# Optimization experiments

Measured on AMD Instinct MI355X. Metric: run time of the kernel, lower is better.

Reference implementation:

```python
import jax, jax.numpy as jnp
import numpy as np

B, S, IN_DIM, OUT_DIM = 4, 2048, 1024, 1024
NEG = -9e15

def _xavier(key, shape, gain=1.414):
    fan_in, fan_out = shape[0], shape[1]
    a = gain * np.sqrt(6.0 / (fan_in + fan_out))
    return jax.random.uniform(key, shape, jnp.float32, -a, a)

def setup_inputs() -> dict:
    key = jax.random.key(0)
    ks = jax.random.split(key, 8)
    x = jax.random.normal(ks[0], (B, S, IN_DIM), jnp.float32)
    W_query = _xavier(ks[1], (IN_DIM, OUT_DIM))
    W_key = _xavier(ks[2], (IN_DIM, OUT_DIM))
    W_value = _xavier(ks[3], (IN_DIM, OUT_DIM))
    # torch Linear default init (kaiming-uniform-ish); values don't matter for correctness baseline
    W1 = _xavier(ks[4], (OUT_DIM + IN_DIM, OUT_DIM), gain=1.0)
    b1 = jnp.zeros((OUT_DIM,), jnp.float32)
    W2 = _xavier(ks[5], (OUT_DIM, OUT_DIM), gain=1.0)
    b2 = jnp.zeros((OUT_DIM,), jnp.float32)
    return {"x": x, "W_query": W_query, "W_key": W_key, "W_value": W_value,
            "W1": W1, "b1": b1, "W2": W2, "b2": b2}

def reference(x, W_query, W_key, W_value, W1, b1, W2, b2):
    # QKV projections: [B,S,in] @ [in,out] -> [B,S,out]
    q = jnp.einsum('bsi,io->bso', x, W_query)
    k = jnp.einsum('bsi,io->bso', x, W_key)
    v = jnp.einsum('bsi,io->bso', x, W_value)
    scale = 1.0 / jnp.sqrt(jnp.float32(OUT_DIM))
    e = jnp.einsum('bqd,bkd->bqk', q, k) * scale  # [B,S,S]
    causal = jnp.tril(jnp.ones((S, S), jnp.float32))  # mask > 0 keeps lower triangle
    attn = jnp.where(causal > 0, e, jnp.float32(NEG))
    attn = jax.nn.softmax(attn, axis=2)
    # dropout: eval mode (train=False) -> identity
    out = jnp.einsum('bqk,bkd->bqd', attn, v)  # [B,S,out]
    h = jnp.concatenate([out, x], axis=-1)  # [B,S,out+in]
    h = jax.nn.relu(jnp.einsum('bsf,fo->bso', h, W1) + b1)
    return jnp.einsum('bsf,fo->bso', h, W2) + b2
```

## Files before the change

kernel.cpp:

```cpp
#include <hip/hip_runtime.h>
#include <stdint.h>

typedef __attribute__((ext_vector_type(8))) short short8;
typedef __attribute__((ext_vector_type(4))) short short4v;
typedef __attribute__((ext_vector_type(4))) float f32x4;

__device__ __forceinline__ unsigned short f32_to_bf16(float f) {
    unsigned int u = __float_as_uint(f);
    u += 0x7FFFu + ((u >> 16) & 1u);
    return (unsigned short)(u >> 16);
}

__device__ __forceinline__ short8 load8_f32_as_bf16(const float* __restrict__ ap) {
    f32x4 f0 = *(const f32x4*)ap;
    f32x4 f1 = *(const f32x4*)(ap + 4);
    union { short8 s; unsigned short u[8]; } cv;
#pragma unroll
    for (int t = 0; t < 4; ++t) {
        cv.u[t]     = f32_to_bf16(f0[t]);
        cv.u[t + 4] = f32_to_bf16(f1[t]);
    }
    return cv.s;
}

__device__ __forceinline__ void gld_lds16(const void* g, void* l) {
    __builtin_amdgcn_global_load_lds(
        (const __attribute__((address_space(1))) unsigned int*)(unsigned long long)(uintptr_t)g,
        (__attribute__((address_space(3))) unsigned int*)(unsigned int)(uintptr_t)l,
        16, 0, 0);
}

template<int MT>
__global__ __launch_bounds__(256, 4)
void gemm128(const unsigned short* __restrict__ A,
             int lda,
             const unsigned short* __restrict__ B, int ldb,
             void* __restrict__ C, int ldc, int K,
             long bStride, long cStride)
{
    int z = blockIdx.z;
    int mblk = blockIdx.x * 8 + (blockIdx.y & 7);
    int nblk = blockIdx.y >> 3;
    int m0 = mblk * MT;
    int n0 = nblk * 128;

    const unsigned short* Ab = A;
    const unsigned short* Bb = B + (size_t)z * bStride;

    __shared__ __align__(16) short As[MT * 64];
    __shared__ __align__(16) short Bs[128 * 64];

    int tid  = threadIdx.x;
    int lane = tid & 63, wid = tid >> 6;
    constexpr int MI = MT / 32;
    int wm = (wid & 1) * (MT / 2), wn = (wid >> 1) * 64;
    int fr = lane & 15, fq = lane >> 4;
    int sw0 = ((fq    ) ^ (fr & 7)) * 16;
    int sw1 = ((fq ^ 4) ^ (fr & 7)) * 16;

    int rS = tid >> 3;
    int cS = ((tid & 7) ^ (rS & 7)) * 8;
    char* AsB = (char*)As; char* BsB = (char*)Bs;

    f32x4 acc[MI][4];
#pragma unroll
    for (int i = 0; i < MI; ++i)
#pragma unroll
    for (int j = 0; j < 4; ++j) acc[i][j] = f32x4{0.f, 0.f, 0.f, 0.f};

    for (int k0 = 0; k0 < K; k0 += 64) {
        const unsigned short* pa = Ab + (size_t)(m0 + rS) * lda + k0 + cS;
        const unsigned short* pb = Bb + (size_t)(n0 + rS) * ldb + k0 + cS;
#pragma unroll
        for (int t = 0; t < MT / 32; ++t)
            gld_lds16(pa + (size_t)(32 * t) * lda, AsB + t * 4096 + tid * 16);
#pragma unroll
        for (int t = 0; t < 4; ++t)
            gld_lds16(pb + (size_t)(32 * t) * ldb,  BsB + t * 4096 + tid * 16);
        __syncthreads();

#pragma unroll
        for (int kh = 0; kh < 2; ++kh) {
            int sw = kh ? sw1 : sw0;
            short8 a[MI], b[4];
#pragma unroll
            for (int i = 0; i < MI; ++i)
                a[i] = *(const short8*)(AsB + (wm + i * 16 + fr) * 128 + sw);
#pragma unroll
            for (int j = 0; j < 4; ++j)
                b[j] = *(const short8*)(BsB + (wn + j * 16 + fr) * 128 + sw);
#pragma unroll
            for (int i = 0; i < MI; ++i)
#pragma unroll
            for (int j = 0; j < 4; ++j)
                acc[i][j] = __builtin_amdgcn_mfma_f32_16x16x32_bf16(a[i], b[j], acc[i][j], 0, 0, 0);
        }
        __syncthreads();
    }

    unsigned short* Cz = (unsigned short*)C + (size_t)z * cStride;
#pragma unroll
    for (int i = 0; i < MI; ++i)
#pragma unroll
    for (int j = 0; j < 4; ++j)
#pragma unroll
    for (int r = 0; r < 4; ++r) {
        int row = m0 + wm + i * 16 + fq * 4 + r;
        int col = n0 + wn + j * 16 + fr;
        Cz[(size_t)row * ldc + col] = f32_to_bf16(acc[i][j][r]);
    }
}

__global__ __launch_bounds__(256, 4)
void scorevt(const unsigned short* __restrict__ q,
             const unsigned short* __restrict__ k,
             unsigned short* __restrict__ S, float* __restrict__ rsum,
             float scale,
             const unsigned short* __restrict__ WvT,
             const unsigned short* __restrict__ xb,
             unsigned short* __restrict__ vT)
{
    int glin = blockIdx.x;
    bool isV = glin >= 544;
    int z = 0, m0, n0;
    const unsigned short *Ab, *Bb;
    if (!isV) {
        int t = (glin & 7) * 68 + (glin >> 3);
        z = t / 136;
        int tri = t - z * 136;
        int a = (int)sqrtf(2.f * (float)tri + 1.f);
        if (a > 15) a = 15;
        while (a < 15 && ((a + 1) * (a + 2) / 2) <= tri) ++a;
        while (a > 0 && (a * (a + 1) / 2) > tri) --a;
        m0 = a * 128;
        n0 = (tri - a * (a + 1) / 2) * 128;
        Ab = q + (size_t)z * 2048 * 1024;
        Bb = k + (size_t)z * 2048 * 1024;
    } else {
        int g2 = glin - 544;
        int xcd = g2 & 7, idx = g2 >> 3;
        int nblk = xcd * 8 + (idx & 7);
        int mblk = idx >> 3;
        m0 = mblk * 128;
        n0 = nblk * 128;
        Ab = WvT;
        Bb = xb;
    }

    __shared__ __align__(16) short As[128 * 64];
    __shared__ __align__(16) short Bs[128 * 64];

    int tid  = threadIdx.x;
    int lane = tid & 63, wid = tid >> 6;
    int wm = (wid & 1) * 64, wn = (wid >> 1) * 64;
    int fr = lane & 15, fq = lane >> 4;
    int sw0 = ((fq    ) ^ (fr & 7)) * 16;
    int sw1 = ((fq ^ 4) ^ (fr & 7)) * 16;

    int rS = tid >> 3;
    int cS = ((tid & 7) ^ (rS & 7)) * 8;
    char* AsB = (char*)As; char* BsB = (char*)Bs;

    f32x4 acc[4][4];
#pragma unroll
    for (int i = 0; i < 4; ++i)
#pragma unroll
    for (int j = 0; j < 4; ++j) acc[i][j] = f32x4{0.f, 0.f, 0.f, 0.f};

    for (int k0 = 0; k0 < 1024; k0 += 64) {
        const unsigned short* pa = Ab + (size_t)(m0 + rS) * 1024 + k0 + cS;
        const unsigned short* pb = Bb + (size_t)(n0 + rS) * 1024 + k0 + cS;
#pragma unroll
        for (int t = 0; t < 4; ++t)
            gld_lds16(pa + (size_t)(32 * t) * 1024, AsB + t * 4096 + tid * 16);
#pragma unroll
        for (int t = 0; t < 4; ++t)
            gld_lds16(pb + (size_t)(32 * t) * 1024, BsB + t * 4096 + tid * 16);
        __syncthreads();

#pragma unroll
        for (int kh = 0; kh < 2; ++kh) {
            int sw = kh ? sw1 : sw0;
            short8 a[4], b[4];
#pragma unroll
            for (int i = 0; i < 4; ++i)
                a[i] = *(const short8*)(AsB + (wm + i * 16 + fr) * 128 + sw);
#pragma unroll
            for (int j = 0; j < 4; ++j)
                b[j] = *(const short8*)(BsB + (wn + j * 16 + fr) * 128 + sw);
#pragma unroll
            for (int i = 0; i < 4; ++i)
#pragma unroll
            for (int j = 0; j < 4; ++j)
                acc[i][j] = __builtin_amdgcn_mfma_f32_16x16x32_bf16(a[i], b[j], acc[i][j], 0, 0, 0);
        }
        __syncthreads();
    }

    if (!isV) {
        unsigned short* Cz = S + (size_t)z * 2048 * 2048;
        float* rs = rsum + (size_t)z * 2048;
#pragma unroll
        for (int i = 0; i < 4; ++i)
#pragma unroll
        for (int r = 0; r < 4; ++r) {
            int row = m0 + wm + i * 16 + fq * 4 + r;
            float s = 0.f;
#pragma unroll
            for (int j = 0; j < 4; ++j) {
                int col = n0 + wn + j * 16 + fr;
                float e = (col <= row) ? __expf(acc[i][j][r] * scale - 16.f) : 0.f;
                s += e;
                Cz[(size_t)row * 2048 + col] = f32_to_bf16(e);
            }
            s += __shfl_xor(s, 1);
            s += __shfl_xor(s, 2);
            s += __shfl_xor(s, 4);
            s += __shfl_xor(s, 8);
            if (fr == 0) atomicAdd(&rs[row], s);
        }
    } else {
#pragma unroll
        for (int i = 0; i < 4; ++i)
#pragma unroll
        for (int j = 0; j < 4; ++j)
#pragma unroll
        for (int r = 0; r < 4; ++r) {
            int row = m0 + wm + i * 16 + fq * 4 + r;
            int col = n0 + wn + j * 16 + fr;
            vT[(size_t)row * 8192 + col] = f32_to_bf16(acc[i][j][r]);
        }
    }
}

__global__ __launch_bounds__(256, 2)
void gemmdb(const unsigned short* __restrict__ A,
            int lda,
            const unsigned short* __restrict__ B, int ldb,
            void* __restrict__ C, int ldc, int K,
            long aStride, long bStride, long cStride,
            const float* __restrict__ bias, long biasStride)
{
    int glin = (int)blockIdx.z * 128 + (int)blockIdx.y * 8 + (int)blockIdx.x;
    int xcd = glin & 7;
    int s   = glin >> 3;
    int z = xcd >> 1;
    int h  = xcd & 1;
    int jm = s & 7;
    int nblk = s >> 3;
    int mblk = (jm & 1) ? (15 - h - (jm >> 1) * 2) : ((jm >> 1) * 2 + h);
    int m0 = mblk * 128;
    int n0 = nblk * 128;

    const unsigned short* Ab = A + (size_t)z * aStride;
    const unsigned short* Bb = B + (size_t)z * bStride;

    __shared__ __align__(16) char lds[65536];

    int tid  = threadIdx.x;
    int lane = tid & 63, wid = tid >> 6;
    int wm = (wid & 1) * 64, wn = (wid >> 1) * 64;
    int fr = lane & 15, fq = lane >> 4;
    int sw0 = ((fq    ) ^ (fr & 7)) * 16;
    int sw1 = ((fq ^ 4) ^ (fr & 7)) * 16;

    int rS = tid >> 3;
    int cS = ((tid & 7) ^ (rS & 7)) * 8;

    int kend = min(K, m0 + 128);
    int NT = kend >> 6;

    f32x4 acc[4][4];
#pragma unroll
    for (int i = 0; i < 4; ++i)
#pragma unroll
    for (int j = 0; j < 4; ++j) acc[i][j] = f32x4{0.f, 0.f, 0.f, 0.f};

    auto STAGE = [&](int kt) {
        char* dst = lds + (kt & 1) * 32768;
        const unsigned short* pa = Ab + (size_t)(m0 + rS) * lda + (kt << 6) + cS;
        const unsigned short* pb = Bb + (size_t)(n0 + rS) * ldb + (kt << 6) + cS;
#pragma unroll
        for (int u = 0; u < 4; ++u)
            gld_lds16(pa + (size_t)(32 * u) * lda, dst + u * 4096 + tid * 16);
#pragma unroll
        for (int u = 0; u < 4; ++u)
            gld_lds16(pb + (size_t)(32 * u) * ldb, dst + 16384 + u * 4096 + tid * 16);
    };

    STAGE(0);
    for (int t = 0; t < NT; ++t) {
        if (t + 1 < NT) {
            STAGE(t + 1);
            asm volatile("s_waitcnt vmcnt(8)" ::: "memory");
        } else {
            asm volatile("s_waitcnt vmcnt(0)" ::: "memory");
        }
        __builtin_amdgcn_s_barrier();
        __builtin_amdgcn_sched_barrier(0);
        const char* AsB = (const char*)lds + (t & 1) * 32768;
        const char* BsB = AsB + 16384;
#pragma unroll
        for (int kh = 0; kh < 2; ++kh) {
            int sw = kh ? sw1 : sw0;
            short8 a[4], b[4];
#pragma unroll
            for (int i = 0; i < 4; ++i)
                a[i] = *(const short8*)(AsB + (wm + i * 16 + fr) * 128 + sw);
#pragma unroll
            for (int j = 0; j < 4; ++j)
                b[j] = *(const short8*)(BsB + (wn + j * 16 + fr) * 128 + sw);
            __builtin_amdgcn_s_setprio(1);
#pragma unroll
            for (int i = 0; i < 4; ++i)
#pragma unroll
            for (int j = 0; j < 4; ++j)
                acc[i][j] = __builtin_amdgcn_mfma_f32_16x16x32_bf16(a[i], b[j], acc[i][j], 0, 0, 0);
            __builtin_amdgcn_s_setprio(0);
        }
        __builtin_amdgcn_s_barrier();
        __builtin_amdgcn_sched_barrier(0);
        asm volatile("" ::: "memory");
    }

    unsigned short* Cz = (unsigned short*)C + (size_t)z * cStride;
#pragma unroll
    for (int i = 0; i < 4; ++i)
#pragma unroll
    for (int r = 0; r < 4; ++r) {
        int row = m0 + wm + i * 16 + fq * 4 + r;
        float inv = 1.f / bias[z * biasStride + row];
#pragma unroll
        for (int j = 0; j < 4; ++j) {
            int col = n0 + wn + j * 16 + fr;
            Cz[(size_t)row * ldc + col] = f32_to_bf16(acc[i][j][r] * inv);
        }
    }
}

template<int AMODE, int EPI>
__global__ __launch_bounds__(512, 2)
void gemm8p(const unsigned short* __restrict__ A, const unsigned short* __restrict__ A2,
            int lda, int lda2, int ksplit,
            const unsigned short* __restrict__ B, int ldb,
            void* __restrict__ C, int ldc, int K,
            const float* __restrict__ bias)
{
    int lin = blockIdx.y * gridDim.x + blockIdx.x;
    int xcd = lin & 7, idx = lin >> 3;
    int mch = (int)gridDim.y >> 3;
    int mblk = xcd * mch + idx % mch;
    int nblk = idx / mch;
    int m0 = mblk * 256, n0 = nblk * 128;

    constexpr int TILE = 49152;
    __shared__ __align__(16) char lds[3 * TILE];

    int tid  = threadIdx.x;
    int lane = tid & 63, wid = tid >> 6;
    int wm = (wid & 3) * 64, wn = (wid >> 2) * 64;
    int fr = lane & 15, fq = lane >> 4;
    int sw0 = ((fq    ) ^ (fr & 7)) * 16;
    int sw1 = ((fq ^ 4) ^ (fr & 7)) * 16;

    int rS = tid >> 3;
    int cS = ((tid & 7) ^ (rS & 7)) * 8;

    int NT = K >> 6;

    f32x4 acc[4][4];
#pragma unroll
    for (int i = 0; i < 4; ++i)
#pragma unroll
    for (int j = 0; j < 4; ++j) acc[i][j] = f32x4{0.f, 0.f, 0.f, 0.f};

    auto STAGE = [&](int t, int slot) {
        int k0 = t << 6;
        char* dst = lds + slot * TILE;
        const unsigned short* Asrc = A; int koff = k0, ldax = lda;
        if (AMODE == 2 && k0 >= ksplit) { Asrc = A2; koff = k0 - ksplit; ldax = lda2; }
        const unsigned short* pa = Asrc + (size_t)(m0 + rS) * ldax + koff + cS;
        const unsigned short* pb = B    + (size_t)(n0 + rS) * ldb  + k0   + cS;
#pragma unroll
        for (int u = 0; u < 4; ++u)
            gld_lds16(pa + (size_t)(64 * u) * ldax, dst + u * 8192 + tid * 16);
#pragma unroll
        for (int u = 0; u < 2; ++u)
            gld_lds16(pb + (size_t)(64 * u) * ldb, dst + 32768 + u * 8192 + tid * 16);
    };

    STAGE(0, 0);
    STAGE(1, 1);
    asm volatile("s_waitcnt vmcnt(6)" ::: "memory");
    __builtin_amdgcn_s_barrier();
    __builtin_amdgcn_sched_barrier(0);
    asm volatile("" ::: "memory");

    int sc = 0, ss = 2;
    for (int t = 0; t < NT; ++t) {
        if (t + 2 < NT) STAGE(t + 2, ss);
        const char* AsB = (const char*)(lds + sc * TILE);
        const char* BsB = AsB + 32768;
#pragma unroll
        for (int kh = 0; kh < 2; ++kh) {
            int sw = kh ? sw1 : sw0;
            short8 a[4], b[4];
#pragma unroll
            for (int i = 0; i < 4; ++i)
                a[i] = *(const short8*)(AsB + (wm + i * 16 + fr) * 128 + sw);
#pragma unroll
            for (int j = 0; j < 4; ++j)
                b[j] = *(const short8*)(BsB + (wn + j * 16 + fr) * 128 + sw);
            __builtin_amdgcn_s_setprio(1);
#pragma unroll
            for (int i = 0; i < 4; ++i)
#pragma unroll
            for (int j = 0; j < 4; ++j)
                acc[i][j] = __builtin_amdgcn_mfma_f32_16x16x32_bf16(a[i], b[j], acc[i][j], 0, 0, 0);
            __builtin_amdgcn_s_setprio(0);
        }
        if (t + 1 < NT) {
            if (t + 2 < NT) { asm volatile("s_waitcnt vmcnt(6)" ::: "memory"); }
            else            { asm volatile("s_waitcnt vmcnt(0)" ::: "memory"); }
            __builtin_amdgcn_s_barrier();
            __builtin_amdgcn_sched_barrier(0);
            asm volatile("" ::: "memory");
        }
        sc = sc == 2 ? 0 : sc + 1;
        ss = ss == 2 ? 0 : ss + 1;
    }

#pragma unroll
    for (int i = 0; i < 4; ++i)
#pragma unroll
    for (int j = 0; j < 4; ++j)
#pragma unroll
    for (int r = 0; r < 4; ++r) {
        int row = m0 + wm + i * 16 + fq * 4 + r;
        int col = n0 + wn + j * 16 + fr;
        float v = acc[i][j][r];
        if (EPI == 2) {
            v += bias[col];
            v = v > 0.f ? v : 0.f;
            ((unsigned short*)C)[(size_t)row * ldc + col] = f32_to_bf16(v);
        } else {
            ((float*)C)[(size_t)row * ldc + col] = v + bias[col];
        }
    }
}

__device__ __forceinline__ void transpose_tile64(const float* __restrict__ in,
                                                 unsigned short* __restrict__ out,
                                                 int rows, int cols, int bx, int by, int tid)
{
    __shared__ float t[64][65];
    int tx = tid & 15, ty = tid >> 4;
    int r0 = by * 64, c0 = bx * 64;
#pragma unroll
    for (int i = 0; i < 4; ++i) {
        f32x4 v = *(const f32x4*)(in + (size_t)(r0 + ty + i * 16) * cols + c0 + tx * 4);
#pragma unroll
        for (int j = 0; j < 4; ++j) t[ty + i * 16][tx * 4 + j] = v[j];
    }
    __syncthreads();
#pragma unroll
    for (int i = 0; i < 4; ++i) {
        union { short4v s; unsigned short u[4]; } o;
#pragma unroll
        for (int j = 0; j < 4; ++j) o.u[j] = f32_to_bf16(t[tx * 4 + j][ty + i * 16]);
        *(short4v*)(out + (size_t)(c0 + ty + i * 16) * rows + r0 + tx * 4) = o.s;
    }
}

__global__ __launch_bounds__(256)
void prep_kernel(const float* __restrict__ x,
                 const float* __restrict__ Wq, const float* __restrict__ Wk,
                 const float* __restrict__ Wv, const float* __restrict__ W1,
                 const float* __restrict__ W2,
                 unsigned short* __restrict__ xb, unsigned short* __restrict__ WT,
                 unsigned short* __restrict__ W1T, unsigned short* __restrict__ W2T,
                 float* __restrict__ rsum)
{
    int idx = blockIdx.x;
    int tid = threadIdx.x;
    if (idx < 1024) {
#pragma unroll
        for (int it = 0; it < 4; ++it) {
            size_t i = ((size_t)idx * 4 + it) * 2048 + (size_t)tid * 8;
            *(short8*)(xb + i) = load8_f32_as_bf16(x + i);
        }
    } else if (idx < 1792) {
        int t = idx - 1024;
        int w = t >> 8; t &= 255;
        const float* in = w == 0 ? Wq : (w == 1 ? Wk : Wv);
        transpose_tile64(in, WT + (size_t)w * 1024 * 1024, 1024, 1024,
                         t & 15, t >> 4, tid);
    } else if (idx < 2304) {
        int t = idx - 1792;
        transpose_tile64(W1, W1T, 2048, 1024, t & 15, t >> 4, tid);
    } else if (idx < 2560) {
        int t = idx - 2304;
        transpose_tile64(W2, W2T, 1024, 1024, t & 15, t >> 4, tid);
    } else {
        int t = idx - 2560;
        f32x4 zero = {0.f, 0.f, 0.f, 0.f};
        float* p = rsum + ((size_t)t * 256 + tid) * 8;
        *(f32x4*)p = zero;
        *(f32x4*)(p + 4) = zero;
    }
}

extern "C" void kernel_launch(void* const* d_in, const int* in_sizes, int n_in,
                              void* d_out, int out_size, void* d_ws, size_t ws_size,
                              hipStream_t stream)
{
    const float* x  = (const float*)d_in[0];
    const float* Wq = (const float*)d_in[1];
    const float* Wk = (const float*)d_in[2];
    const float* Wv = (const float*)d_in[3];
    const float* W1 = (const float*)d_in[4];
    const float* b1 = (const float*)d_in[5];
    const float* W2 = (const float*)d_in[6];
    const float* b2 = (const float*)d_in[7];
    float* out = (float*)d_out;

    size_t off = 0;
    auto alloc = [&](size_t bytes) {
        char* r = (char*)d_ws + off;
        off += (bytes + 255) & ~(size_t)255;
        return r;
    };
    const size_t TOK = (size_t)8192 * 1024;
    unsigned short* WT   = (unsigned short*)alloc((size_t)3072 * 1024 * 2);
    unsigned short* W1T  = (unsigned short*)alloc((size_t)1024 * 2048 * 2);
    unsigned short* W2T  = (unsigned short*)alloc((size_t)1024 * 1024 * 2);
    unsigned short* xb   = (unsigned short*)alloc(TOK * 2);
    unsigned short* vT   = (unsigned short*)alloc((size_t)1024 * 8192 * 2);
    unsigned short* attn = (unsigned short*)alloc(TOK * 2);
    float*          rsum = (float*)         alloc((size_t)4 * 2048 * 4);
    unsigned short* q    = (unsigned short*)alloc(TOK * 2);
    unsigned short* k    = (unsigned short*)alloc(TOK * 2);
    unsigned short* S    = (unsigned short*)alloc((size_t)4 * 2048 * 2048 * 2);
    unsigned short* h1   = S;

    prep_kernel<<<2564, 256, 0, stream>>>(x, Wq, Wk, Wv, W1, W2, xb, WT, W1T, W2T, rsum);

    gemm128<128><<<dim3(8, 64, 2), 256, 0, stream>>>(
        xb, 1024, WT, 1024, q, 1024, 1024,
        (long)1024 * 1024, (long)TOK);

    scorevt<<<1056, 256, 0, stream>>>(
        q, k, S, rsum, 0.03125f, WT + (size_t)2 * 1024 * 1024, xb, vT);

    gemmdb<<<dim3(8, 16, 4), 256, 0, stream>>>(
        S, 2048, vT, 8192, attn, 1024, 2048,
        (long)2048 * 2048, (long)2048, (long)2048 * 1024, rsum, 2048);

    gemm8p<2, 2><<<dim3(8, 32, 1), 512, 0, stream>>>(
        attn, xb, 1024, 1024, 1024, W1T, 2048, h1, 1024, 2048, b1);

    gemm8p<0, 3><<<dim3(8, 32, 1), 512, 0, stream>>>(
        h1, nullptr, 1024, 0, 0, W2T, 1024, out, 1024, 1024, b2);
}
```

Before: 277.6 us.

## Co-schedule x·W1 half with PV GEMM and move W1/W2 transposes into score kernel

Splits the first MLP GEMM so that the x-part (x·W1[1024:]) runs in the same launch as the causal PV GEMM, interleaving blocks to fill idle CUs left by the triangular workload. Its result, plus bias, goes to an fp32 buffer that the attn·W1 GEMM adds in its epilogue. The W1/W2 transposes move from the prep kernel into extra blocks of the score kernel. This costs an extra fp32 intermediate write and read, and the PV path loses its double-buffered pipelined loop for a simpler single-buffer one.

```diff
diff --git a/kernel.cpp b/kernel.cpp
--- a/kernel.cpp
+++ b/kernel.cpp
@@ -28,6 +28,29 @@
         (const __attribute__((address_space(1))) unsigned int*)(unsigned long long)(uintptr_t)g,
         (__attribute__((address_space(3))) unsigned int*)(unsigned int)(uintptr_t)l,
         16, 0, 0);
+}
+
+__device__ __forceinline__ void transpose_tile64(const float* __restrict__ in,
+                                                 unsigned short* __restrict__ out,
+                                                 int rows, int cols, int bx, int by,
+                                                 int tid, float* __restrict__ tt)
+{
+    int tx = tid & 15, ty = tid >> 4;
+    int r0 = by * 64, c0 = bx * 64;
+#pragma unroll
+    for (int i = 0; i < 4; ++i) {
+        f32x4 v = *(const f32x4*)(in + (size_t)(r0 + ty + i * 16) * cols + c0 + tx * 4);
+#pragma unroll
+        for (int j = 0; j < 4; ++j) tt[(ty + i * 16) * 65 + tx * 4 + j] = v[j];
+    }
+    __syncthreads();
+#pragma unroll
+    for (int i = 0; i < 4; ++i) {
+        union { short4v s; unsigned short u[4]; } o;
+#pragma unroll
+        for (int j = 0; j < 4; ++j) o.u[j] = f32_to_bf16(tt[(tx * 4 + j) * 65 + ty + i * 16]);
+        *(short4v*)(out + (size_t)(c0 + ty + i * 16) * rows + r0 + tx * 4) = o.s;
+    }
 }
 
 template<int MT>
@@ -112,15 +135,28 @@
 }
 
 __global__ __launch_bounds__(256, 4)
-void scorevt(const unsigned short* __restrict__ q,
-             const unsigned short* __restrict__ k,
-             unsigned short* __restrict__ S, float* __restrict__ rsum,
-             float scale,
-             const unsigned short* __restrict__ WvT,
-             const unsigned short* __restrict__ xb,
-             unsigned short* __restrict__ vT)
-{
+void scorevt2(const unsigned short* __restrict__ q,
+              const unsigned short* __restrict__ k,
+              unsigned short* __restrict__ S, float* __restrict__ rsum,
+              float scale,
+              const unsigned short* __restrict__ WvT,
+              const unsigned short* __restrict__ xb,
+              unsigned short* __restrict__ vT,
+              const float* __restrict__ W1, unsigned short* __restrict__ W1T,
+              const float* __restrict__ W2, unsigned short* __restrict__ W2T)
+{
+    __shared__ __align__(16) char smem[32768];
     int glin = blockIdx.x;
+    int tid = threadIdx.x;
+
+    if (glin >= 1056) {
+        int t = glin - 1056;
+        float* tt = (float*)smem;
+        if (t < 512) transpose_tile64(W1, W1T, 2048, 1024, t & 15, t >> 4, tid, tt);
+        else { t -= 512; transpose_tile64(W2, W2T, 1024, 1024, t & 15, t >> 4, tid, tt); }
+        return;
+    }
+
     bool isV = glin >= 544;
     int z = 0, m0, n0;
     const unsigned short *Ab, *Bb;
@@ -147,10 +183,9 @@
         Bb = xb;
     }
 
-    __shared__ __align__(16) short As[128 * 64];
-    __shared__ __align__(16) short Bs[128 * 64];
-
-    int tid  = threadIdx.x;
+    short* As = (short*)smem;
+    short* Bs = (short*)(smem + 16384);
+
     int lane = tid & 63, wid = tid >> 6;
     int wm = (wid & 1) * 64, wn = (wid >> 1) * 64;
     int fr = lane & 15, fq = lane >> 4;
@@ -233,29 +268,47 @@
     }
 }
 
-__global__ __launch_bounds__(256, 2)
-void gemmdb(const unsigned short* __restrict__ A,
-            int lda,
-            const unsigned short* __restrict__ B, int ldb,
-            void* __restrict__ C, int ldc, int K,
-            long aStride, long bStride, long cStride,
-            const float* __restrict__ bias, long biasStride)
-{
-    int glin = (int)blockIdx.z * 128 + (int)blockIdx.y * 8 + (int)blockIdx.x;
-    int xcd = glin & 7;
-    int s   = glin >> 3;
-    int z = xcd >> 1;
-    int h  = xcd & 1;
-    int jm = s & 7;
-    int nblk = s >> 3;
-    int mblk = (jm & 1) ? (15 - h - (jm >> 1) * 2) : ((jm >> 1) * 2 + h);
-    int m0 = mblk * 128;
-    int n0 = nblk * 128;
-
-    const unsigned short* Ab = A + (size_t)z * aStride;
-    const unsigned short* Bb = B + (size_t)z * bStride;
-
-    __shared__ __align__(16) char lds[65536];
+__global__ __launch_bounds__(256, 4)
+void pvx(const unsigned short* __restrict__ S,
+         const unsigned short* __restrict__ vT,
+         unsigned short* __restrict__ attn,
+         const float* __restrict__ rsum,
+         const unsigned short* __restrict__ xb,
+         const unsigned short* __restrict__ W1T,
+         float* __restrict__ h1pre,
+         const float* __restrict__ b1)
+{
+    int glin = blockIdx.x;
+    bool isPV = (glin & 1) == 0;
+    int g2 = glin >> 1;
+    int z = 0, m0, n0, kend, lda, ldb;
+    const unsigned short *Ab, *Bb;
+    if (isPV) {
+        int xcd = g2 & 7;
+        int s   = g2 >> 3;
+        z = xcd >> 1;
+        int h  = xcd & 1;
+        int jm = s & 7;
+        int nblk = s >> 3;
+        int mblk = (jm & 1) ? (15 - h - (jm >> 1) * 2) : ((jm >> 1) * 2 + h);
+        m0 = mblk * 128;
+        n0 = nblk * 128;
+        kend = m0 + 128;
+        Ab = S + (size_t)z * 2048 * 2048;  lda = 2048;
+        Bb = vT + (size_t)z * 2048;        ldb = 8192;
+    } else {
+        int xcd = g2 & 7, idx = g2 >> 3;
+        int mblk = xcd * 8 + (idx & 7);
+        int nblk = idx >> 3;
+        m0 = mblk * 128;
+        n0 = nblk * 128;
+        kend = 1024;
+        Ab = xb;            lda = 1024;
+        Bb = W1T + 1024;    ldb = 2048;
+    }
+
+    __shared__ __align__(16) short As[128 * 64];
+    __shared__ __align__(16) short Bs[128 * 64];
 
     int tid  = threadIdx.x;
     int lane = tid & 63, wid = tid >> 6;
@@ -266,9 +319,7 @@
 
     int rS = tid >> 3;
     int cS = ((tid & 7) ^ (rS & 7)) * 8;
-
-    int kend = min(K, m0 + 128);
-    int NT = kend >> 6;
+    char* AsB = (char*)As; char* BsB = (char*)Bs;
 
     f32x4 acc[4][4];
 #pragma unroll
@@ -276,30 +327,17 @@
 #pragma unroll
     for (int j = 0; j < 4; ++j) acc[i][j] = f32x4{0.f, 0.f, 0.f, 0.f};
 
-    auto STAGE = [&](int kt) {
-        char* dst = lds + (kt & 1) * 32768;
-        const unsigned short* pa = Ab + (size_t)(m0 + rS) * lda + (kt << 6) + cS;
-        const unsigned short* pb = Bb + (size_t)(n0 + rS) * ldb + (kt << 6) + cS;
-#pragma unroll
-        for (int u = 0; u < 4; ++u)
-            gld_lds16(pa + (size_t)(32 * u) * lda, dst + u * 4096 + tid * 16);
-#pragma unroll
-        for (int u = 0; u < 4; ++u)
-            gld_lds16(pb + (size_t)(32 * u) * ldb, dst + 16384 + u * 4096 + tid * 16);
-    };
-
-    STAGE(0);
-    for (int t = 0; t < NT; ++t) {
-        if (t + 1 < NT) {
-            STAGE(t + 1);
-            asm volatile("s_waitcnt vmcnt(8)" ::: "memory");
-        } else {
-            asm volatile("s_waitcnt vmcnt(0)" ::: "memory");
-        }
-        __builtin_amdgcn_s_barrier();
-        __builtin_amdgcn_sched_barrier(0);
-        const char* AsB = (const char*)lds + (t & 1) * 32768;
-        const char* BsB = AsB + 16384;
+    for (int k0 = 0; k0 < kend; k0 += 64) {
+        const unsigned short* pa = Ab + (size_t)(m0 + rS) * lda + k0 + cS;
+        const unsigned short* pb = Bb + (size_t)(n0 + rS) * ldb + k0 + cS;
+#pragma unroll
+        for (int t = 0; t < 4; ++t)
+            gld_lds16(pa + (size_t)(32 * t) * lda, AsB + t * 4096 + tid * 16);
+#pragma unroll
+        for (int t = 0; t < 4; ++t)
+            gld_lds16(pb + (size_t)(32 * t) * ldb, BsB + t * 4096 + tid * 16);
+        __syncthreads();
+
 #pragma unroll
         for (int kh = 0; kh < 2; ++kh) {
             int sw = kh ? sw1 : sw0;
@@ -310,38 +348,48 @@
 #pragma unroll
             for (int j = 0; j < 4; ++j)
                 b[j] = *(const short8*)(BsB + (wn + j * 16 + fr) * 128 + sw);
-            __builtin_amdgcn_s_setprio(1);
 #pragma unroll
             for (int i = 0; i < 4; ++i)
 #pragma unroll
             for (int j = 0; j < 4; ++j)
                 acc[i][j] = __builtin_amdgcn_mfma_f32_16x16x32_bf16(a[i], b[j], acc[i][j], 0, 0, 0);
-            __builtin_amdgcn_s_setprio(0);
-        }
-        __builtin_amdgcn_s_barrier();
-        __builtin_amdgcn_sched_barrier(0);
-        asm volatile("" ::: "memory");
-    }
-
-    unsigned short* Cz = (unsigned short*)C + (size_t)z * cStride;
-#pragma unroll
-    for (int i = 0; i < 4; ++i)
-#pragma unroll
-    for (int r = 0; r < 4; ++r) {
-        int row = m0 + wm + i * 16 + fq * 4 + r;
-        float inv = 1.f / bias[z * biasStride + row];
-#pragma unroll
-        for (int j = 0; j < 4; ++j) {
+        }
+        __syncthreads();
+    }
+
+    if (isPV) {
+        unsigned short* Cz = attn + (size_t)z * 2048 * 1024;
+        const float* rs = rsum + (size_t)z * 2048;
+#pragma unroll
+        for (int i = 0; i < 4; ++i)
+#pragma unroll
+        for (int r = 0; r < 4; ++r) {
+            int row = m0 + wm + i * 16 + fq * 4 + r;
+            float inv = 1.f / rs[row];
+#pragma unroll
+            for (int j = 0; j < 4; ++j) {
+                int col = n0 + wn + j * 16 + fr;
+                Cz[(size_t)row * 1024 + col] = f32_to_bf16(acc[i][j][r] * inv);
+            }
+        }
+    } else {
+#pragma unroll
+        for (int i = 0; i < 4; ++i)
+#pragma unroll
+        for (int j = 0; j < 4; ++j)
+#pragma unroll
+        for (int r = 0; r < 4; ++r) {
+            int row = m0 + wm + i * 16 + fq * 4 + r;
             int col = n0 + wn + j * 16 + fr;
-            Cz[(size_t)row * ldc + col] = f32_to_bf16(acc[i][j][r] * inv);
-        }
-    }
-}
-
-template<int AMODE, int EPI>
+            h1pre[(size_t)row * 1024 + col] = acc[i][j][r] + b1[col];
+        }
+    }
+}
+
+template<int EPI>
 __global__ __launch_bounds__(512, 2)
-void gemm8p(const unsigned short* __restrict__ A, const unsigned short* __restrict__ A2,
-            int lda, int lda2, int ksplit,
+void gemm8p(const unsigned short* __restrict__ A,
+            int lda,
             const unsigned short* __restrict__ B, int ldb,
             void* __restrict__ C, int ldc, int K,
             const float* __restrict__ bias)
@@ -377,13 +425,11 @@
     auto STAGE = [&](int t, int slot) {
         int k0 = t << 6;
         char* dst = lds + slot * TILE;
-        const unsigned short* Asrc = A; int koff = k0, ldax = lda;
-        if (AMODE == 2 && k0 >= ksplit) { Asrc = A2; koff = k0 - ksplit; ldax = lda2; }
-        const unsigned short* pa = Asrc + (size_t)(m0 + rS) * ldax + koff + cS;
-        const unsigned short* pb = B    + (size_t)(n0 + rS) * ldb  + k0   + cS;
+        const unsigned short* pa = A + (size_t)(m0 + rS) * lda + k0 + cS;
+        const unsigned short* pb = B + (size_t)(n0 + rS) * ldb + k0 + cS;
 #pragma unroll
         for (int u = 0; u < 4; ++u)
-            gld_lds16(pa + (size_t)(64 * u) * ldax, dst + u * 8192 + tid * 16);
+            gld_lds16(pa + (size_t)(64 * u) * lda, dst + u * 8192 + tid * 16);
 #pragma unroll
         for (int u = 0; u < 2; ++u)
             gld_lds16(pb + (size_t)(64 * u) * ldb, dst + 32768 + u * 8192 + tid * 16);
@@ -439,8 +485,8 @@
         int row = m0 + wm + i * 16 + fq * 4 + r;
         int col = n0 + wn + j * 16 + fr;
         float v = acc[i][j][r];
-        if (EPI == 2) {
-            v += bias[col];
+        if (EPI == 5) {
+            v += bias[(size_t)row * 1024 + col];
             v = v > 0.f ? v : 0.f;
             ((unsigned short*)C)[(size_t)row * ldc + col] = f32_to_bf16(v);
         } else {
@@ -449,38 +495,14 @@
     }
 }
 
-__device__ __forceinline__ void transpose_tile64(const float* __restrict__ in,
-                                                 unsigned short* __restrict__ out,
-                                                 int rows, int cols, int bx, int by, int tid)
-{
-    __shared__ float t[64][65];
-    int tx = tid & 15, ty = tid >> 4;
-    int r0 = by * 64, c0 = bx * 64;
-#pragma unroll
-    for (int i = 0; i < 4; ++i) {
-        f32x4 v = *(const f32x4*)(in + (size_t)(r0 + ty + i * 16) * cols + c0 + tx * 4);
-#pragma unroll
-        for (int j = 0; j < 4; ++j) t[ty + i * 16][tx * 4 + j] = v[j];
-    }
-    __syncthreads();
-#pragma unroll
-    for (int i = 0; i < 4; ++i) {
-        union { short4v s; unsigned short u[4]; } o;
-#pragma unroll
-        for (int j = 0; j < 4; ++j) o.u[j] = f32_to_bf16(t[tx * 4 + j][ty + i * 16]);
-        *(short4v*)(out + (size_t)(c0 + ty + i * 16) * rows + r0 + tx * 4) = o.s;
-    }
-}
-
 __global__ __launch_bounds__(256)
 void prep_kernel(const float* __restrict__ x,
                  const float* __restrict__ Wq, const float* __restrict__ Wk,
-                 const float* __restrict__ Wv, const float* __restrict__ W1,
-                 const float* __restrict__ W2,
+                 const float* __restrict__ Wv,
                  unsigned short* __restrict__ xb, unsigned short* __restrict__ WT,
-                 unsigned short* __restrict__ W1T, unsigned short* __restrict__ W2T,
                  float* __restrict__ rsum)
 {
+    __shared__ __align__(16) char smem[16704];
     int idx = blockIdx.x;
     int tid = threadIdx.x;
     if (idx < 1024) {
@@ -494,15 +516,9 @@
         int w = t >> 8; t &= 255;
         const float* in = w == 0 ? Wq : (w == 1 ? Wk : Wv);
         transpose_tile64(in, WT + (size_t)w * 1024 * 1024, 1024, 1024,
-                         t & 15, t >> 4, tid);
-    } else if (idx < 2304) {
+                         t & 15, t >> 4, tid, (float*)smem);
+    } else {
         int t = idx - 1792;
-        transpose_tile64(W1, W1T, 2048, 1024, t & 15, t >> 4, tid);
-    } else if (idx < 2560) {
-        int t = idx - 2304;
-        transpose_tile64(W2, W2T, 1024, 1024, t & 15, t >> 4, tid);
-    } else {
-        int t = idx - 2560;
         f32x4 zero = {0.f, 0.f, 0.f, 0.f};
         float* p = rsum + ((size_t)t * 256 + tid) * 8;
         *(f32x4*)p = zero;
@@ -542,23 +558,23 @@
     unsigned short* k    = (unsigned short*)alloc(TOK * 2);
     unsigned short* S    = (unsigned short*)alloc((size_t)4 * 2048 * 2048 * 2);
     unsigned short* h1   = S;
-
-    prep_kernel<<<2564, 256, 0, stream>>>(x, Wq, Wk, Wv, W1, W2, xb, WT, W1T, W2T, rsum);
+    float*          h1pre = (float*)q;
+
+    prep_kernel<<<1796, 256, 0, stream>>>(x, Wq, Wk, Wv, xb, WT, rsum);
 
     gemm128<128><<<dim3(8, 64, 2), 256, 0, stream>>>(
         xb, 1024, WT, 1024, q, 1024, 1024,
         (long)1024 * 1024, (long)TOK);
 
-    scorevt<<<1056, 256, 0, stream>>>(
-        q, k, S, rsum, 0.03125f, WT + (size_t)2 * 1024 * 1024, xb, vT);
-
-    gemmdb<<<dim3(8, 16, 4), 256, 0, stream>>>(
-        S, 2048, vT, 8192, attn, 1024, 2048,
-        (long)2048 * 2048, (long)2048, (long)2048 * 1024, rsum, 2048);
-
-    gemm8p<2, 2><<<dim3(8, 32, 1), 512, 0, stream>>>(
-        attn, xb, 1024, 1024, 1024, W1T, 2048, h1, 1024, 2048, b1);
-
-    gemm8p<0, 3><<<dim3(8, 32, 1), 512, 0, stream>>>(
-        h1, nullptr, 1024, 0, 0, W2T, 1024, out, 1024, 1024, b2);
-}
+    scorevt2<<<1824, 256, 0, stream>>>(
+        q, k, S, rsum, 0.03125f, WT + (size_t)2 * 1024 * 1024, xb, vT,
+        W1, W1T, W2, W2T);
+
+    pvx<<<1024, 256, 0, stream>>>(S, vT, attn, rsum, xb, W1T, h1pre, b1);
+
+    gemm8p<5><<<dim3(8, 32, 1), 512, 0, stream>>>(
+        attn, 1024, W1T, 2048, h1, 1024, 1024, h1pre);
+
+    gemm8p<3><<<dim3(8, 32, 1), 512, 0, stream>>>(
+        h1, 1024, W2T, 1024, out, 1024, 1024, b2);
+}
```

Result: slower. 297.3 us (+7.1%).
